# Optimization experiments

Measured on AMD Instinct MI355X. Metric: run time of the kernel, lower is better.

The kernel has to match this reference:

```python
import jax, jax.numpy as jnp
import numpy as np

NUM_HEADS = 16
EMB = 1024
V_IN = 512
V_OUT = 1024


def setup_inputs() -> dict:
    key = jax.random.key(0)
    ks = jax.random.split(key, 11)
    s = 0.02
    return {
        "query": jax.random.normal(ks[0], (8, 512, EMB), jnp.float32),
        "key": jax.random.normal(ks[1], (8, 1024, V_IN), jnp.float32),
        "value": jax.random.normal(ks[2], (8, 1024, V_IN), jnp.float32),
        "Wq": jax.random.normal(ks[3], (EMB, EMB), jnp.float32) * s,
        "bq": jax.random.normal(ks[4], (EMB,), jnp.float32) * s,
        "Wk": jax.random.normal(ks[5], (V_IN, EMB), jnp.float32) * s,
        "bk": jax.random.normal(ks[6], (EMB,), jnp.float32) * s,
        "Wv": jax.random.normal(ks[7], (V_IN, V_OUT), jnp.float32) * s,
        "bv": jax.random.normal(ks[8], (V_OUT,), jnp.float32) * s,
        "Wo": jax.random.normal(ks[9], (V_OUT, EMB), jnp.float32) * s,
        "bo": jax.random.normal(ks[10], (EMB,), jnp.float32) * s,
    }


def reference(query, key, value, Wq, bq, Wk, bk, Wv, bv, Wo, bo):
    B, Lq, _ = query.shape
    Lk = key.shape[1]
    H = NUM_HEADS
    dh = EMB // H          # 64, key/query head dim (used as softmax scale)
    dv = V_OUT // H        # 64, value head dim
    q = (query @ Wq + bq).reshape(B, Lq, H, dh)   # [B,Lq,H,dh]
    k = (key @ Wk + bk).reshape(B, Lk, H, dh)     # [B,Lk,H,dh]
    v = (value @ Wv + bv).reshape(B, Lk, H, dv)   # [B,Lk,H,dv]
    scale = 1.0 / np.sqrt(dh).astype(np.float32)
    scores = jnp.einsum('bqhd,bkhd->bhqk', q * scale, k)  # [B,H,Lq,Lk]
    attn = jax.nn.softmax(scores, axis=-1)
    ctx = jnp.einsum('bhqk,bkhd->bqhd', attn, v).reshape(B, Lq, V_OUT)
    return ctx @ Wo + bo  # [B,Lq,EMB]
```

## Files before the change

### kernel.cpp

```cpp
#include <hip/hip_runtime.h>
#include <hip/hip_bf16.h>

#define EMB  1024
#define VIN  512
#define VOUT 1024
#define NH   16
#define DH   64
#define BB   8
#define LQ   512
#define LK   1024

typedef __attribute__((ext_vector_type(8))) short bf16x8;
typedef __attribute__((ext_vector_type(4))) float f32x4;

typedef const __attribute__((address_space(1))) unsigned int* gptr_t;
typedef __attribute__((address_space(3))) unsigned int* lptr_t;

__device__ __forceinline__ unsigned short f2bf(float x) {
    unsigned int u = __float_as_uint(x);
    u += 0x7FFF + ((u >> 16) & 1);
    return (unsigned short)(u >> 16);
}
__device__ __forceinline__ float bf2f(unsigned short h) {
    return __uint_as_float(((unsigned int)h) << 16);
}
__device__ __forceinline__ float fexp2(float x) {
    return __builtin_amdgcn_exp2f(x);
}
__device__ __forceinline__ unsigned int pk2bf(float a, float b) {
    float2 f; f.x = a; f.y = b;
    __hip_bfloat162 t = __float22bfloat162_rn(f);
    return *reinterpret_cast<unsigned int*>(&t);
}

#define SWZ(row, cb) (((row) << 7) + ((cb) ^ (((row) & 7) << 4)))

__global__ __launch_bounds__(256) void asplit3(const float* __restrict__ q,
                                               const float* __restrict__ k,
                                               const float* __restrict__ v,
                                               unsigned short* __restrict__ Aq,
                                               unsigned short* __restrict__ Ak,
                                               unsigned short* __restrict__ Av)
{
    const int which = blockIdx.x >> 12;
    const float* in = (which == 0) ? q : (which == 1) ? k : v;
    unsigned short* out = (which == 0) ? Aq : (which == 1) ? Ak : Av;
    const int i = (blockIdx.x & 4095) * 256 + threadIdx.x;
    float val[4];
    *reinterpret_cast<float4*>(val) = *reinterpret_cast<const float4*>(&in[(size_t)i * 4]);
    unsigned short h[4];
#pragma unroll
    for (int j = 0; j < 4; ++j) h[j] = f2bf(val[j]);
    *reinterpret_cast<uint2*>(&out[(size_t)i * 4]) = *reinterpret_cast<uint2*>(h);
}

__device__ __forceinline__ void wtile(const float* W, unsigned short* Wht,
                                      unsigned short* Wlt, int K, int N,
                                      int bx, int by, int tx, int ty)
{
    __shared__ float t[32][33];
    const int n0 = bx * 32, k0 = by * 32;
#pragma unroll
    for (int r = 0; r < 32; r += 8)
        t[ty + r][tx] = W[(size_t)(k0 + ty + r) * N + n0 + tx];
    __syncthreads();
#pragma unroll
    for (int r = 0; r < 32; r += 8) {
        float x = t[tx][ty + r];
        unsigned short h = f2bf(x);
        size_t o = (size_t)(n0 + ty + r) * K + k0 + tx;
        Wht[o] = h;
        if (Wlt) Wlt[o] = f2bf(x - bf2f(h));
    }
}

__global__ __launch_bounds__(256) void wsplit_all(const float* __restrict__ Wq,
                                                  const float* __restrict__ Wk,
                                                  const float* __restrict__ Wv,
                                                  const float* __restrict__ Wo,
                                                  unsigned short* __restrict__ Wqt,
                                                  unsigned short* __restrict__ Wkt,
                                                  unsigned short* __restrict__ Wvt,
                                                  unsigned short* __restrict__ Woh,
                                                  unsigned short* __restrict__ Wol)
{
    const int id = blockIdx.x;
    const int tx = threadIdx.x, ty = threadIdx.y;
    if (id < 1024)       wtile(Wq, Wqt, nullptr, 1024, 1024, id & 31, id >> 5, tx, ty);
    else if (id < 1536)  wtile(Wk, Wkt, nullptr, 512, 1024, (id - 1024) & 31, (id - 1024) >> 5, tx, ty);
    else if (id < 2048)  wtile(Wv, Wvt, nullptr, 512, 1024, (id - 1536) & 31, (id - 1536) >> 5, tx, ty);
    else                 wtile(Wo, Woh, Wol, 1024, 1024, (id - 2048) & 31, (id - 2048) >> 5, tx, ty);
}

__device__ __forceinline__ void stagehalf(const unsigned short* g0, int Kstride,
                                          unsigned short* l0, int lane)
{
#pragma unroll
    for (int r = 0; r < 8; ++r) {
        int row  = r * 8 + (lane >> 3);
        int colb = ((lane & 7) << 4) ^ ((row & 7) << 4);
        const unsigned short* src = g0 + (size_t)row * Kstride + (colb >> 1);
        __builtin_amdgcn_global_load_lds((gptr_t)src, (lptr_t)(l0 + r * 512), 16, 0, 0);
    }
}

template<int EPI>
__global__ __launch_bounds__(256, 2) void gemm1(const unsigned short* __restrict__ Ah,
                                                const unsigned short* __restrict__ Bht,
                                                const float* __restrict__ bias,
                                                unsigned short* __restrict__ Ch,
                                                int M, int N, int K)
{
    __shared__ unsigned short As[2][128 * 64], Bs[2][128 * 64];

    const int nbx = N >> 7;
    const int nwg = gridDim.x;
    const int qq  = nwg >> 3;
    const int id  = blockIdx.x;
    const int swz = (id & 7) * qq + (id >> 3);
    const int bx = swz % nbx, by = swz / nbx;
    const int m0 = by * 128, n0 = bx * 128;

    const int tid  = threadIdx.x;
    const int lane = tid & 63;
    const int w    = tid >> 6;
    const int wm = (w & 1) * 64;
    const int wn = (w >> 1) * 64;
    const int lr = lane & 15;
    const int lk = lane >> 4;

    f32x4 acc[4][4];
#pragma unroll
    for (int i = 0; i < 4; ++i)
#pragma unroll
        for (int j = 0; j < 4; ++j) acc[i][j] = (f32x4)(0.f);

    const unsigned short* mysrc = (w < 2)
        ? Ah  + (size_t)(m0 + (w & 1) * 64) * K
        : Bht + (size_t)(n0 + (w & 1) * 64) * K;
    const int lofs = (w & 1) * 4096;
    unsigned short* pl0 = ((w < 2) ? As[0] : Bs[0]) + lofs;
    unsigned short* pl1 = ((w < 2) ? As[1] : Bs[1]) + lofs;

    stagehalf(mysrc, K, pl0, lane);

    const int nt = K >> 6;
    for (int t = 0; t < nt; ++t) {
        __syncthreads();
        if (t + 1 < nt)
            stagehalf(mysrc + ((size_t)(t + 1) << 6), K, ((t & 1) ? pl0 : pl1), lane);

        const char* Ac = (const char*)As[t & 1];
        const char* Bc = (const char*)Bs[t & 1];
#pragma unroll
        for (int ks = 0; ks < 2; ++ks) {
            bf16x8 ah[4], bh[4];
            const int cb = ks * 64 + lk * 16;
#pragma unroll
            for (int f = 0; f < 4; ++f) {
                ah[f] = *reinterpret_cast<const bf16x8*>(Ac + SWZ(wm + f * 16 + lr, cb));
                bh[f] = *reinterpret_cast<const bf16x8*>(Bc + SWZ(wn + f * 16 + lr, cb));
            }
#pragma unroll
            for (int fm = 0; fm < 4; ++fm)
#pragma unroll
                for (int fn = 0; fn < 4; ++fn)
                    acc[fm][fn] = __builtin_amdgcn_mfma_f32_16x16x32_bf16(ah[fm], bh[fn], acc[fm][fn], 0, 0, 0);
        }
    }

#pragma unroll
    for (int fn = 0; fn < 4; ++fn) {
        const int col = n0 + wn + fn * 16 + lr;
        const float bv = bias[col];
#pragma unroll
        for (int fm = 0; fm < 4; ++fm) {
            const int row0 = m0 + wm + fm * 16 + lk * 4;
            if constexpr (EPI == 1) {
#pragma unroll
                for (int r = 0; r < 4; ++r)
                    Ch[(size_t)(row0 + r) * N + col] = f2bf(acc[fm][fn][r] + bv);
            } else if constexpr (EPI == 3) {
#pragma unroll
                for (int r = 0; r < 4; ++r)
                    Ch[(size_t)(row0 + r) * N + col] = f2bf((acc[fm][fn][r] + bv) * 0.18033688011112042f);
            } else {
                unsigned short h4[4];
#pragma unroll
                for (int r = 0; r < 4; ++r)
                    h4[r] = f2bf(acc[fm][fn][r] + bv);
                size_t o = (((size_t)((row0 >> 10) * NH + (col >> 6)) * 64 + (col & 63)) << 10) + (row0 & 1023);
                *reinterpret_cast<uint2*>(&Ch[o]) = *reinterpret_cast<uint2*>(h4);
            }
        }
    }
}

__device__ __forceinline__ void stageplane(const unsigned short* g0, int Kstride,
                                           unsigned short* l0, int lane)
{
#pragma unroll
    for (int r = 0; r < 16; ++r) {
        int row  = r * 8 + (lane >> 3);
        int colb = ((lane & 7) << 4) ^ ((row & 7) << 4);
        const unsigned short* src = g0 + (size_t)row * Kstride + (colb >> 1);
        __builtin_amdgcn_global_load_lds((gptr_t)src, (lptr_t)(l0 + r * 512), 16, 0, 0);
    }
}

__global__ __launch_bounds__(256) void gemm2(const unsigned short* __restrict__ Ah,
                                             const unsigned short* __restrict__ Al,
                                             const unsigned short* __restrict__ Bht,
                                             const unsigned short* __restrict__ Blt,
                                             const float* __restrict__ bias,
                                             float* __restrict__ C,
                                             int M, int N, int K)
{
    __shared__ unsigned short As_h[2][128 * 64], As_l[2][128 * 64];
    __shared__ unsigned short Bs_h[2][128 * 64], Bs_l[2][128 * 64];

    const int nbx = N >> 7;
    const int nwg = gridDim.x;
    const int qq  = nwg >> 3;
    const int id  = blockIdx.x;
    const int swz = (id & 7) * qq + (id >> 3);
    const int bx = swz % nbx, by = swz / nbx;
    const int m0 = by * 128, n0 = bx * 128;

    const int tid  = threadIdx.x;
    const int lane = tid & 63;
    const int w    = tid >> 6;
    const int wm = (w & 1) * 64;
    const int wn = (w >> 1) * 64;
    const int lr = lane & 15;
    const int lk = lane >> 4;

    f32x4 acc[4][4];
#pragma unroll
    for (int i = 0; i < 4; ++i)
#pragma unroll
        for (int j = 0; j < 4; ++j) acc[i][j] = (f32x4)(0.f);

    const unsigned short* mysrc =
        (w == 0) ? Ah + (size_t)m0 * K :
        (w == 1) ? Al + (size_t)m0 * K :
        (w == 2) ? Bht + (size_t)n0 * K :
                   Blt + (size_t)n0 * K;
    unsigned short* pl0 = (w == 0) ? As_h[0] : (w == 1) ? As_l[0] : (w == 2) ? Bs_h[0] : Bs_l[0];
    unsigned short* pl1 = (w == 0) ? As_h[1] : (w == 1) ? As_l[1] : (w == 2) ? Bs_h[1] : Bs_l[1];

    stageplane(mysrc, K, pl0, lane);

    const int nt = K >> 6;
    for (int t = 0; t < nt; ++t) {
        __syncthreads();
        if (t + 1 < nt)
            stageplane(mysrc + ((size_t)(t + 1) << 6), K, ((t & 1) ? pl0 : pl1), lane);

        const char* Ahc = (const char*)As_h[t & 1];
        const char* Alc = (const char*)As_l[t & 1];
        const char* Bhc = (const char*)Bs_h[t & 1];
        const char* Blc = (const char*)Bs_l[t & 1];
#pragma unroll
        for (int ks = 0; ks < 2; ++ks) {
            bf16x8 ah[4], al[4], bh[4], bl[4];
            const int cb = ks * 64 + lk * 16;
#pragma unroll
            for (int f = 0; f < 4; ++f) {
                int rowA = wm + f * 16 + lr;
                ah[f] = *reinterpret_cast<const bf16x8*>(Ahc + SWZ(rowA, cb));
                al[f] = *reinterpret_cast<const bf16x8*>(Alc + SWZ(rowA, cb));
                int rowB = wn + f * 16 + lr;
                bh[f] = *reinterpret_cast<const bf16x8*>(Bhc + SWZ(rowB, cb));
                bl[f] = *reinterpret_cast<const bf16x8*>(Blc + SWZ(rowB, cb));
            }
#pragma unroll
            for (int fm = 0; fm < 4; ++fm)
#pragma unroll
                for (int fn = 0; fn < 4; ++fn) {
                    acc[fm][fn] = __builtin_amdgcn_mfma_f32_16x16x32_bf16(ah[fm], bh[fn], acc[fm][fn], 0, 0, 0);
                    acc[fm][fn] = __builtin_amdgcn_mfma_f32_16x16x32_bf16(ah[fm], bl[fn], acc[fm][fn], 0, 0, 0);
                    acc[fm][fn] = __builtin_amdgcn_mfma_f32_16x16x32_bf16(al[fm], bh[fn], acc[fm][fn], 0, 0, 0);
                }
        }
    }

#pragma unroll
    for (int fn = 0; fn < 4; ++fn) {
        const int col = n0 + wn + fn * 16 + lr;
        const float bv = bias[col];
#pragma unroll
        for (int fm = 0; fm < 4; ++fm) {
            const int row0 = m0 + wm + fm * 16 + lk * 4;
#pragma unroll
            for (int r = 0; r < 4; ++r)
                C[(size_t)(row0 + r) * N + col] = acc[fm][fn][r] + bv;
        }
    }
}

__device__ __forceinline__ void stage32(const unsigned short* g0, unsigned short* l0, int lane)
{
#pragma unroll
    for (int r = 0; r < 4; ++r) {
        int row  = r * 8 + (lane >> 3);
        int colb = ((lane & 7) << 4) ^ ((row & 7) << 4);
        const unsigned short* src = g0 + ((size_t)row << 10) + (colb >> 1);
        __builtin_amdgcn_global_load_lds((gptr_t)src, (lptr_t)(l0 + r * 512), 16, 0, 0);
    }
}

__global__ __launch_bounds__(256, 4) void attn_mfma(const unsigned short* __restrict__ Qh,
                                                    const unsigned short* __restrict__ Kh,
                                                    const unsigned short* __restrict__ Vth,
                                                    unsigned short* __restrict__ Ch,
                                                    unsigned short* __restrict__ Cl)
{
    const int id  = blockIdx.x;
    const int qt  = (id >> 3) & 7;
    const int grp = (id & 7) | ((id >> 6) << 3);
    const int h = grp & 15, b = grp >> 4;

    const int tid  = threadIdx.x;
    const int lane = tid & 63;
    const int w    = tid >> 6;
    const int lr   = lane & 15;
    const int lk   = lane >> 4;

    __shared__ unsigned short KVs[2][2][4096];
    __shared__ unsigned short Ps[4][1024];

    bf16x8 qb[2];
    {
        const unsigned short* qrow = &Qh[(size_t)(b * LQ + qt * 64 + w * 16 + lr) * EMB + h * DH];
        qb[0] = *reinterpret_cast<const bf16x8*>(qrow + lk * 8);
        qb[1] = *reinterpret_cast<const bf16x8*>(qrow + 32 + lk * 8);
    }

    const unsigned short* K0 = Kh + ((size_t)(b * LK) << 10) + h * DH;
    const unsigned short* V0 = Vth + ((size_t)(grp * 64) << 10);

    {
        const int half = (w & 1) * 32;
        if (w < 2) stage32(K0 + ((size_t)half << 10), KVs[0][0] + half * 64, lane);
        else       stage32(V0 + ((size_t)half << 10), KVs[0][1] + half * 64, lane);
    }

    float m = -1e30f, lsum = 0.f;
    f32x4 acc[4];
#pragma unroll
    for (int f = 0; f < 4; ++f) acc[f] = (f32x4)(0.f);

    for (int kt = 0; kt < LK / 64; ++kt) {
        const int cur = kt & 1;
        __syncthreads();

        if (kt + 1 < LK / 64) {
            const size_t koff = (size_t)(kt + 1) * 64;
            const int half = (w & 1) * 32;
            if (w < 2) stage32(K0 + ((koff + half) << 10), KVs[cur ^ 1][0] + half * 64, lane);
            else       stage32(V0 + ((size_t)half << 10) + koff, KVs[cur ^ 1][1] + half * 64, lane);
        }

        const char* Ks = (const char*)KVs[cur][0];
        const char* Vs = (const char*)KVs[cur][1];

        f32x4 s[4];
#pragma unroll
        for (int fn = 0; fn < 4; ++fn) s[fn] = (f32x4)(0.f);
        __builtin_amdgcn_s_setprio(1);
#pragma unroll
        for (int ks = 0; ks < 2; ++ks) {
            const int cb = ks * 64 + lk * 16;
#pragma unroll
            for (int fn = 0; fn < 4; ++fn) {
                bf16x8 kb = *reinterpret_cast<const bf16x8*>(Ks + SWZ(fn * 16 + lr, cb));
                s[fn] = __builtin_amdgcn_mfma_f32_16x16x32_bf16(kb, qb[ks], s[fn], 0, 0, 0);
            }
        }
        __builtin_amdgcn_s_setprio(0);

        {
            f32x4 t4 = s[0];
#pragma unroll
            for (int fn = 1; fn < 4; ++fn)
#pragma unroll
                for (int r = 0; r < 4; ++r) t4[r] = fmaxf(t4[r], s[fn][r]);
            float mx = fmaxf(fmaxf(t4[0], t4[1]), fmaxf(t4[2], t4[3]));
            mx = fmaxf(mx, __shfl_xor(mx, 16));
            mx = fmaxf(mx, __shfl_xor(mx, 32));

            if (!__all(mx <= m + 8.f)) {
                float mnew = fmaxf(m, mx);
                float corr = fexp2(m - mnew);
                m = mnew;
                lsum *= corr;
#pragma unroll
                for (int f = 0; f < 4; ++f)
#pragma unroll
                    for (int r = 0; r < 4; ++r) acc[f][r] *= corr;
            }
            float rs = 0.f;
#pragma unroll
            for (int fn = 0; fn < 4; ++fn)
#pragma unroll
                for (int r = 0; r < 4; ++r) {
                    float p = fexp2(s[fn][r] - m);
                    s[fn][r] = p;
                    rs += p;
                }
            rs += __shfl_xor(rs, 16);
            rs += __shfl_xor(rs, 32);
            lsum += rs;
        }

#pragma unroll
        for (int fn = 0; fn < 4; ++fn) {
            uint2 pk;
            pk.x = pk2bf(s[fn][0], s[fn][1]);
            pk.y = pk2bf(s[fn][2], s[fn][3]);
            *reinterpret_cast<uint2*>((char*)Ps[w] + SWZ(lr, fn * 32 + lk * 8)) = pk;
        }

        __builtin_amdgcn_s_setprio(1);
#pragma unroll
        for (int ks = 0; ks < 2; ++ks) {
            const int cb = ks * 64 + lk * 16;
            bf16x8 pa = *reinterpret_cast<const bf16x8*>((char*)Ps[w] + SWZ(lr, cb));
#pragma unroll
            for (int f = 0; f < 4; ++f) {
                bf16x8 vb = *reinterpret_cast<const bf16x8*>(Vs + SWZ(f * 16 + lr, cb));
                acc[f] = __builtin_amdgcn_mfma_f32_16x16x32_bf16(vb, pa, acc[f], 0, 0, 0);
            }
        }
        __builtin_amdgcn_s_setprio(0);
    }

    {
        float inv = 1.f / lsum;
        const size_t row = (size_t)(b * LQ + qt * 64 + w * 16 + lr);
#pragma unroll
        for (int f = 0; f < 4; ++f)
#pragma unroll
            for (int r = 0; r < 4; ++r) {
                float x = acc[f][r] * inv;
                unsigned short hh = f2bf(x);
                size_t o = (row << 10) + h * DH + f * 16 + lk * 4 + r;
                Ch[o] = hh;
                Cl[o] = f2bf(x - bf2f(hh));
            }
    }
}

extern "C" void kernel_launch(void* const* d_in, const int* in_sizes, int n_in,
                              void* d_out, int out_size, void* d_ws, size_t ws_size,
                              hipStream_t stream)
{
    const float* query = (const float*)d_in[0];
    const float* key   = (const float*)d_in[1];
    const float* value = (const float*)d_in[2];
    const float* Wq = (const float*)d_in[3];
    const float* bq = (const float*)d_in[4];
    const float* Wk = (const float*)d_in[5];
    const float* bk = (const float*)d_in[6];
    const float* Wv = (const float*)d_in[7];
    const float* bv = (const float*)d_in[8];
    const float* Wo = (const float*)d_in[9];
    const float* bo = (const float*)d_in[10];
    float* out = (float*)d_out;

    unsigned short* Qh  = (unsigned short*)d_ws;
    unsigned short* Kh  = Qh  + (size_t)4194304;
    unsigned short* Vth = Kh  + (size_t)8388608;
    unsigned short* Aq  = Vth + (size_t)8388608;
    unsigned short* Ak  = Aq  + (size_t)4194304;
    unsigned short* Av  = Ak  + (size_t)4194304;
    unsigned short* Ch  = Av  + (size_t)4194304;
    unsigned short* Cl  = Ch  + (size_t)4194304;
    unsigned short* Wqt = Cl  + (size_t)4194304;
    unsigned short* Wkt = Wqt + (size_t)1048576;
    unsigned short* Wvt = Wkt + (size_t)524288;
    unsigned short* Woh = Wvt + (size_t)524288;
    unsigned short* Wol = Woh + (size_t)1048576;

    asplit3<<<12288, 256, 0, stream>>>(query, key, value, Aq, Ak, Av);
    wsplit_all<<<3072, dim3(32, 8), 0, stream>>>(Wq, Wk, Wv, Wo, Wqt, Wkt, Wvt, Woh, Wol);

    gemm1<3><<<(EMB / 128) * (BB * LQ / 128), 256, 0, stream>>>(Aq, Wqt, bq, Qh, BB * LQ, EMB, EMB);
    gemm1<1><<<(EMB / 128) * (BB * LK / 128), 256, 0, stream>>>(Ak, Wkt, bk, Kh, BB * LK, EMB, VIN);
    gemm1<2><<<(VOUT / 128) * (BB * LK / 128), 256, 0, stream>>>(Av, Wvt, bv, Vth, BB * LK, VOUT, VIN);

    attn_mfma<<<LQ / 64 * NH * BB, 256, 0, stream>>>(Qh, Kh, Vth, Ch, Cl);

    gemm2<<<(EMB / 128) * (BB * LQ / 128), 256, 0, stream>>>(Ch, Cl, Woh, Wol, bo, out, BB * LQ, EMB, VOUT);
}
```

Before: 133.7 us.

## Merge conversion kernels and fuse Q/K/V projection GEMMs into single launches

Merges the activation bf16 conversion and the weight transpose/split into one kernel, and combines the three Q/K/V projection GEMM launches into one grouped launch of 1280 workgroups that picks its segment from the block index. This removes launch overhead and the tail underfill between the separate grids. It also moves the cross-lane max shuffles in the attention softmax inside the rare rescale branch, so the common path skips them. The cost is runtime segment selection and branching in the epilogue instead of compile-time templates.

```diff
diff --git a/kernel.cpp b/kernel.cpp
--- a/kernel.cpp
+++ b/kernel.cpp
@@ -35,25 +35,6 @@
 
 #define SWZ(row, cb) (((row) << 7) + ((cb) ^ (((row) & 7) << 4)))
 
-__global__ __launch_bounds__(256) void asplit3(const float* __restrict__ q,
-                                               const float* __restrict__ k,
-                                               const float* __restrict__ v,
-                                               unsigned short* __restrict__ Aq,
-                                               unsigned short* __restrict__ Ak,
-                                               unsigned short* __restrict__ Av)
-{
-    const int which = blockIdx.x >> 12;
-    const float* in = (which == 0) ? q : (which == 1) ? k : v;
-    unsigned short* out = (which == 0) ? Aq : (which == 1) ? Ak : Av;
-    const int i = (blockIdx.x & 4095) * 256 + threadIdx.x;
-    float val[4];
-    *reinterpret_cast<float4*>(val) = *reinterpret_cast<const float4*>(&in[(size_t)i * 4]);
-    unsigned short h[4];
-#pragma unroll
-    for (int j = 0; j < 4; ++j) h[j] = f2bf(val[j]);
-    *reinterpret_cast<uint2*>(&out[(size_t)i * 4]) = *reinterpret_cast<uint2*>(h);
-}
-
 __device__ __forceinline__ void wtile(const float* W, unsigned short* Wht,
                                       unsigned short* Wlt, int K, int N,
                                       int bx, int by, int tx, int ty)
@@ -74,22 +55,42 @@
     }
 }
 
-__global__ __launch_bounds__(256) void wsplit_all(const float* __restrict__ Wq,
-                                                  const float* __restrict__ Wk,
-                                                  const float* __restrict__ Wv,
-                                                  const float* __restrict__ Wo,
-                                                  unsigned short* __restrict__ Wqt,
-                                                  unsigned short* __restrict__ Wkt,
-                                                  unsigned short* __restrict__ Wvt,
-                                                  unsigned short* __restrict__ Woh,
-                                                  unsigned short* __restrict__ Wol)
+__global__ __launch_bounds__(256) void convert_all(const float* __restrict__ q,
+                                                   const float* __restrict__ k,
+                                                   const float* __restrict__ v,
+                                                   const float* __restrict__ Wq,
+                                                   const float* __restrict__ Wk,
+                                                   const float* __restrict__ Wv,
+                                                   const float* __restrict__ Wo,
+                                                   unsigned short* __restrict__ Aq,
+                                                   unsigned short* __restrict__ Ak,
+                                                   unsigned short* __restrict__ Av,
+                                                   unsigned short* __restrict__ Wqt,
+                                                   unsigned short* __restrict__ Wkt,
+                                                   unsigned short* __restrict__ Wvt,
+                                                   unsigned short* __restrict__ Woh,
+                                                   unsigned short* __restrict__ Wol)
 {
     const int id = blockIdx.x;
-    const int tx = threadIdx.x, ty = threadIdx.y;
-    if (id < 1024)       wtile(Wq, Wqt, nullptr, 1024, 1024, id & 31, id >> 5, tx, ty);
-    else if (id < 1536)  wtile(Wk, Wkt, nullptr, 512, 1024, (id - 1024) & 31, (id - 1024) >> 5, tx, ty);
-    else if (id < 2048)  wtile(Wv, Wvt, nullptr, 512, 1024, (id - 1536) & 31, (id - 1536) >> 5, tx, ty);
-    else                 wtile(Wo, Woh, Wol, 1024, 1024, (id - 2048) & 31, (id - 2048) >> 5, tx, ty);
+    if (id < 12288) {
+        const int which = id >> 12;
+        const float* in = (which == 0) ? q : (which == 1) ? k : v;
+        unsigned short* out = (which == 0) ? Aq : (which == 1) ? Ak : Av;
+        const int i = (id & 4095) * 256 + threadIdx.x;
+        float val[4];
+        *reinterpret_cast<float4*>(val) = *reinterpret_cast<const float4*>(&in[(size_t)i * 4]);
+        unsigned short h[4];
+#pragma unroll
+        for (int j = 0; j < 4; ++j) h[j] = f2bf(val[j]);
+        *reinterpret_cast<uint2*>(&out[(size_t)i * 4]) = *reinterpret_cast<uint2*>(h);
+    } else {
+        const int wid = id - 12288;
+        const int tx = threadIdx.x & 31, ty = threadIdx.x >> 5;
+        if (wid < 1024)      wtile(Wq, Wqt, nullptr, 1024, 1024, wid & 31, wid >> 5, tx, ty);
+        else if (wid < 1536) wtile(Wk, Wkt, nullptr, 512, 1024, (wid - 1024) & 31, (wid - 1024) >> 5, tx, ty);
+        else if (wid < 2048) wtile(Wv, Wvt, nullptr, 512, 1024, (wid - 1536) & 31, (wid - 1536) >> 5, tx, ty);
+        else                 wtile(Wo, Woh, Wol, 1024, 1024, (wid - 2048) & 31, (wid - 2048) >> 5, tx, ty);
+    }
 }
 
 __device__ __forceinline__ void stagehalf(const unsigned short* g0, int Kstride,
@@ -104,14 +105,134 @@
     }
 }
 
-template<int EPI>
-__global__ __launch_bounds__(256, 2) void gemm1(const unsigned short* __restrict__ Ah,
-                                                const unsigned short* __restrict__ Bht,
-                                                const float* __restrict__ bias,
-                                                unsigned short* __restrict__ Ch,
-                                                int M, int N, int K)
+__global__ __launch_bounds__(256, 2) void gemm_qkv(const unsigned short* __restrict__ Aq,
+                                                   const unsigned short* __restrict__ Ak,
+                                                   const unsigned short* __restrict__ Av,
+                                                   const unsigned short* __restrict__ Wqt,
+                                                   const unsigned short* __restrict__ Wkt,
+                                                   const unsigned short* __restrict__ Wvt,
+                                                   const float* __restrict__ bq,
+                                                   const float* __restrict__ bk,
+                                                   const float* __restrict__ bv,
+                                                   unsigned short* __restrict__ Qh,
+                                                   unsigned short* __restrict__ Kh,
+                                                   unsigned short* __restrict__ Vth)
 {
     __shared__ unsigned short As[2][128 * 64], Bs[2][128 * 64];
+
+    const int id  = blockIdx.x;
+    const int seg = (id < 256) ? 0 : (id < 768) ? 1 : 2;
+    const int lid = id - ((seg == 0) ? 0 : (seg == 1) ? 256 : 768);
+    const int nwg = (seg == 0) ? 256 : 512;
+    const int K   = (seg == 0) ? 1024 : 512;
+    const unsigned short* Ah  = (seg == 0) ? Aq : (seg == 1) ? Ak : Av;
+    const unsigned short* Bht = (seg == 0) ? Wqt : (seg == 1) ? Wkt : Wvt;
+    const float* bias = (seg == 0) ? bq : (seg == 1) ? bk : bv;
+    unsigned short* Ch = (seg == 0) ? Qh : (seg == 1) ? Kh : Vth;
+    const int N = 1024;
+
+    const int qq  = nwg >> 3;
+    const int swz = (lid & 7) * qq + (lid >> 3);
+    const int bx = swz & 7, by = swz >> 3;
+    const int m0 = by * 128, n0 = bx * 128;
+
+    const int tid  = threadIdx.x;
+    const int lane = tid & 63;
+    const int w    = tid >> 6;
+    const int wm = (w & 1) * 64;
+    const int wn = (w >> 1) * 64;
+    const int lr = lane & 15;
+    const int lk = lane >> 4;
+
+    f32x4 acc[4][4];
+#pragma unroll
+    for (int i = 0; i < 4; ++i)
+#pragma unroll
+        for (int j = 0; j < 4; ++j) acc[i][j] = (f32x4)(0.f);
+
+    const unsigned short* mysrc = (w < 2)
+        ? Ah  + (size_t)(m0 + (w & 1) * 64) * K
+        : Bht + (size_t)(n0 + (w & 1) * 64) * K;
+    const int lofs = (w & 1) * 4096;
+    unsigned short* pl0 = ((w < 2) ? As[0] : Bs[0]) + lofs;
+    unsigned short* pl1 = ((w < 2) ? As[1] : Bs[1]) + lofs;
+
+    stagehalf(mysrc, K, pl0, lane);
+
+    const int nt = K >> 6;
+    for (int t = 0; t < nt; ++t) {
+        __syncthreads();
+        if (t + 1 < nt)
+            stagehalf(mysrc + ((size_t)(t + 1) << 6), K, ((t & 1) ? pl0 : pl1), lane);
+
+        const char* Ac = (const char*)As[t & 1];
+        const char* Bc = (const char*)Bs[t & 1];
+#pragma unroll
+        for (int ks = 0; ks < 2; ++ks) {
+            bf16x8 ah[4], bh[4];
+            const int cb = ks * 64 + lk * 16;
+#pragma unroll
+            for (int f = 0; f < 4; ++f) {
+                ah[f] = *reinterpret_cast<const bf16x8*>(Ac + SWZ(wm + f * 16 + lr, cb));
+                bh[f] = *reinterpret_cast<const bf16x8*>(Bc + SWZ(wn + f * 16 + lr, cb));
+            }
+#pragma unroll
+            for (int fm = 0; fm < 4; ++fm)
+#pragma unroll
+                for (int fn = 0; fn < 4; ++fn)
+                    acc[fm][fn] = __builtin_amdgcn_mfma_f32_16x16x32_bf16(ah[fm], bh[fn], acc[fm][fn], 0, 0, 0);
+        }
+    }
+
+#pragma unroll
+    for (int fn = 0; fn < 4; ++fn) {
+        const int col = n0 + wn + fn * 16 + lr;
+        const float bv_ = bias[col];
+#pragma unroll
+        for (int fm = 0; fm < 4; ++fm) {
+            const int row0 = m0 + wm + fm * 16 + lk * 4;
+            if (seg == 0) {
+#pragma unroll
+                for (int r = 0; r < 4; ++r)
+                    Ch[(size_t)(row0 + r) * N + col] = f2bf((acc[fm][fn][r] + bv_) * 0.18033688011112042f);
+            } else if (seg == 1) {
+#pragma unroll
+                for (int r = 0; r < 4; ++r)
+                    Ch[(size_t)(row0 + r) * N + col] = f2bf(acc[fm][fn][r] + bv_);
+            } else {
+                unsigned short h4[4];
+#pragma unroll
+                for (int r = 0; r < 4; ++r)
+                    h4[r] = f2bf(acc[fm][fn][r] + bv_);
+                size_t o = (((size_t)((row0 >> 10) * NH + (col >> 6)) * 64 + (col & 63)) << 10) + (row0 & 1023);
+                *reinterpret_cast<uint2*>(&Ch[o]) = *reinterpret_cast<uint2*>(h4);
+            }
+        }
+    }
+}
+
+__device__ __forceinline__ void stageplane(const unsigned short* g0, int Kstride,
+                                           unsigned short* l0, int lane)
+{
+#pragma unroll
+    for (int r = 0; r < 16; ++r) {
+        int row  = r * 8 + (lane >> 3);
+        int colb = ((lane & 7) << 4) ^ ((row & 7) << 4);
+        const unsigned short* src = g0 + (size_t)row * Kstride + (colb >> 1);
+        __builtin_amdgcn_global_load_lds((gptr_t)src, (lptr_t)(l0 + r * 512), 16, 0, 0);
+    }
+}
+
+__global__ __launch_bounds__(256) void gemm2(const unsigned short* __restrict__ Ah,
+                                             const unsigned short* __restrict__ Al,
+                                             const unsigned short* __restrict__ Bht,
+                                             const unsigned short* __restrict__ Blt,
+                                             const float* __restrict__ bias,
+                                             float* __restrict__ C,
+                                             int M, int N, int K)
+{
+    __shared__ unsigned short As_h[2][128 * 64], As_l[2][128 * 64];
+    __shared__ unsigned short Bs_h[2][128 * 64], Bs_l[2][128 * 64];
 
     const int nbx = N >> 7;
     const int nwg = gridDim.x;
@@ -135,112 +256,6 @@
 #pragma unroll
         for (int j = 0; j < 4; ++j) acc[i][j] = (f32x4)(0.f);
 
-    const unsigned short* mysrc = (w < 2)
-        ? Ah  + (size_t)(m0 + (w & 1) * 64) * K
-        : Bht + (size_t)(n0 + (w & 1) * 64) * K;
-    const int lofs = (w & 1) * 4096;
-    unsigned short* pl0 = ((w < 2) ? As[0] : Bs[0]) + lofs;
-    unsigned short* pl1 = ((w < 2) ? As[1] : Bs[1]) + lofs;
-
-    stagehalf(mysrc, K, pl0, lane);
-
-    const int nt = K >> 6;
-    for (int t = 0; t < nt; ++t) {
-        __syncthreads();
-        if (t + 1 < nt)
-            stagehalf(mysrc + ((size_t)(t + 1) << 6), K, ((t & 1) ? pl0 : pl1), lane);
-
-        const char* Ac = (const char*)As[t & 1];
-        const char* Bc = (const char*)Bs[t & 1];
-#pragma unroll
-        for (int ks = 0; ks < 2; ++ks) {
-            bf16x8 ah[4], bh[4];
-            const int cb = ks * 64 + lk * 16;
-#pragma unroll
-            for (int f = 0; f < 4; ++f) {
-                ah[f] = *reinterpret_cast<const bf16x8*>(Ac + SWZ(wm + f * 16 + lr, cb));
-                bh[f] = *reinterpret_cast<const bf16x8*>(Bc + SWZ(wn + f * 16 + lr, cb));
-            }
-#pragma unroll
-            for (int fm = 0; fm < 4; ++fm)
-#pragma unroll
-                for (int fn = 0; fn < 4; ++fn)
-                    acc[fm][fn] = __builtin_amdgcn_mfma_f32_16x16x32_bf16(ah[fm], bh[fn], acc[fm][fn], 0, 0, 0);
-        }
-    }
-
-#pragma unroll
-    for (int fn = 0; fn < 4; ++fn) {
-        const int col = n0 + wn + fn * 16 + lr;
-        const float bv = bias[col];
-#pragma unroll
-        for (int fm = 0; fm < 4; ++fm) {
-            const int row0 = m0 + wm + fm * 16 + lk * 4;
-            if constexpr (EPI == 1) {
-#pragma unroll
-                for (int r = 0; r < 4; ++r)
-                    Ch[(size_t)(row0 + r) * N + col] = f2bf(acc[fm][fn][r] + bv);
-            } else if constexpr (EPI == 3) {
-#pragma unroll
-                for (int r = 0; r < 4; ++r)
-                    Ch[(size_t)(row0 + r) * N + col] = f2bf((acc[fm][fn][r] + bv) * 0.18033688011112042f);
-            } else {
-                unsigned short h4[4];
-#pragma unroll
-                for (int r = 0; r < 4; ++r)
-                    h4[r] = f2bf(acc[fm][fn][r] + bv);
-                size_t o = (((size_t)((row0 >> 10) * NH + (col >> 6)) * 64 + (col & 63)) << 10) + (row0 & 1023);
-                *reinterpret_cast<uint2*>(&Ch[o]) = *reinterpret_cast<uint2*>(h4);
-            }
-        }
-    }
-}
-
-__device__ __forceinline__ void stageplane(const unsigned short* g0, int Kstride,
-                                           unsigned short* l0, int lane)
-{
-#pragma unroll
-    for (int r = 0; r < 16; ++r) {
-        int row  = r * 8 + (lane >> 3);
-        int colb = ((lane & 7) << 4) ^ ((row & 7) << 4);
-        const unsigned short* src = g0 + (size_t)row * Kstride + (colb >> 1);
-        __builtin_amdgcn_global_load_lds((gptr_t)src, (lptr_t)(l0 + r * 512), 16, 0, 0);
-    }
-}
-
-__global__ __launch_bounds__(256) void gemm2(const unsigned short* __restrict__ Ah,
-                                             const unsigned short* __restrict__ Al,
-                                             const unsigned short* __restrict__ Bht,
-                                             const unsigned short* __restrict__ Blt,
-                                             const float* __restrict__ bias,
-                                             float* __restrict__ C,
-                                             int M, int N, int K)
-{
-    __shared__ unsigned short As_h[2][128 * 64], As_l[2][128 * 64];
-    __shared__ unsigned short Bs_h[2][128 * 64], Bs_l[2][128 * 64];
-
-    const int nbx = N >> 7;
-    const int nwg = gridDim.x;
-    const int qq  = nwg >> 3;
-    const int id  = blockIdx.x;
-    const int swz = (id & 7) * qq + (id >> 3);
-    const int bx = swz % nbx, by = swz / nbx;
-    const int m0 = by * 128, n0 = bx * 128;
-
-    const int tid  = threadIdx.x;
-    const int lane = tid & 63;
-    const int w    = tid >> 6;
-    const int wm = (w & 1) * 64;
-    const int wn = (w >> 1) * 64;
-    const int lr = lane & 15;
-    const int lk = lane >> 4;
-
-    f32x4 acc[4][4];
-#pragma unroll
-    for (int i = 0; i < 4; ++i)
-#pragma unroll
-        for (int j = 0; j < 4; ++j) acc[i][j] = (f32x4)(0.f);
-
     const unsigned short* mysrc =
         (w == 0) ? Ah + (size_t)m0 * K :
         (w == 1) ? Al + (size_t)m0 * K :
@@ -386,11 +401,11 @@
             for (int fn = 1; fn < 4; ++fn)
 #pragma unroll
                 for (int r = 0; r < 4; ++r) t4[r] = fmaxf(t4[r], s[fn][r]);
-            float mx = fmaxf(fmaxf(t4[0], t4[1]), fmaxf(t4[2], t4[3]));
-            mx = fmaxf(mx, __shfl_xor(mx, 16));
-            mx = fmaxf(mx, __shfl_xor(mx, 32));
-
-            if (!__all(mx <= m + 8.f)) {
+            float lmx = fmaxf(fmaxf(t4[0], t4[1]), fmaxf(t4[2], t4[3]));
+
+            if (!__all(lmx <= m + 8.f)) {
+                float mx = fmaxf(lmx, __shfl_xor(lmx, 16));
+                mx = fmaxf(mx, __shfl_xor(mx, 32));
                 float mnew = fmaxf(m, mx);
                 float corr = fexp2(m - mnew);
                 m = mnew;
@@ -483,12 +498,9 @@
     unsigned short* Woh = Wvt + (size_t)524288;
     unsigned short* Wol = Woh + (size_t)1048576;
 
-    asplit3<<<12288, 256, 0, stream>>>(query, key, value, Aq, Ak, Av);
-    wsplit_all<<<3072, dim3(32, 8), 0, stream>>>(Wq, Wk, Wv, Wo, Wqt, Wkt, Wvt, Woh, Wol);
-
-    gemm1<3><<<(EMB / 128) * (BB * LQ / 128), 256, 0, stream>>>(Aq, Wqt, bq, Qh, BB * LQ, EMB, EMB);
-    gemm1<1><<<(EMB / 128) * (BB * LK / 128), 256, 0, stream>>>(Ak, Wkt, bk, Kh, BB * LK, EMB, VIN);
-    gemm1<2><<<(VOUT / 128) * (BB * LK / 128), 256, 0, stream>>>(Av, Wvt, bv, Vth, BB * LK, VOUT, VIN);
+    convert_all<<<15360, 256, 0, stream>>>(query, key, value, Wq, Wk, Wv, Wo,
+                                           Aq, Ak, Av, Wqt, Wkt, Wvt, Woh, Wol);
+    gemm_qkv<<<1280, 256, 0, stream>>>(Aq, Ak, Av, Wqt, Wkt, Wvt, bq, bk, bv, Qh, Kh, Vth);
 
     attn_mfma<<<LQ / 64 * NH * BB, 256, 0, stream>>>(Qh, Kh, Vth, Ch, Cl);
 
```

New measurement: 122.2 us. 1.09x faster.
